# Kernel tuning notes

Measured on AMD Instinct MI355X. Metric: run time of the kernel, lower is better.

## Reference

```python
import jax, jax.numpy as jnp
import numpy as np

NUM_HEADS = 16
HEAD_DIM = 128
NUM_KV_HEADS = 8
NUM_KV_GROUPS = 2
HIDDEN = 2048
SCALE = 0.5  # hardcoded in the original SDPA call


def _fixed_sincos_pos(E, H):
    # matches ReusedProjReconstructor._fixed_sincos_pos (H even here)
    half = H // 2
    freq = jnp.exp(-jnp.log(jnp.float32(10000.0)) * jnp.arange(half, dtype=jnp.float32) / half)
    pos = jnp.arange(E, dtype=jnp.float32)[:, None]
    ang = pos * freq[None, :]
    return jnp.concatenate([jnp.sin(ang), jnp.cos(ang)], axis=1)  # [E, H]


def setup_inputs() -> dict:
    key = jax.random.key(0)
    ks = jax.random.split(key, 8)
    B, M, H = 4, 2048, HIDDEN
    kv_dim = NUM_KV_HEADS * HEAD_DIM
    s = 0.02
    return {
        "mem_act": jax.random.normal(ks[0], (B, M, H), jnp.float32),
        "Wq": jax.random.normal(ks[1], (H, H), jnp.float32) * s,
        "bq": jax.random.normal(ks[2], (H,), jnp.float32) * s,
        "Wk": jax.random.normal(ks[3], (kv_dim, H), jnp.float32) * s,
        "bk": jax.random.normal(ks[4], (kv_dim,), jnp.float32) * s,
        "Wv": jax.random.normal(ks[5], (kv_dim, H), jnp.float32) * s,
        "bv": jax.random.normal(ks[6], (kv_dim,), jnp.float32) * s,
        "Wo": jax.random.normal(ks[7], (H, H), jnp.float32) * s,
        "E": 2048,
    }


def reference(mem_act, Wq, bq, Wk, bk, Wv, bv, Wo, E):
    B, M, H = mem_act.shape
    # positional query hidden, shared across batch (q_ln is Identity)
    q_hidden = _fixed_sincos_pos(E, H).astype(mem_act.dtype)  # [E, H]
    q = (q_hidden @ Wq.T + bq).reshape(E, NUM_HEADS, HEAD_DIM)          # [E, nh, hd]
    k = (mem_act @ Wk.T + bk).reshape(B, M, NUM_KV_HEADS, HEAD_DIM)     # [B, M, nkv, hd]
    v = (mem_act @ Wv.T + bv).reshape(B, M, NUM_KV_HEADS, HEAD_DIM)
    # GQA: repeat kv heads (repeat_interleave over head dim)
    k = jnp.repeat(k, NUM_KV_GROUPS, axis=2)  # [B, M, nh, hd]
    v = jnp.repeat(v, NUM_KV_GROUPS, axis=2)
    # non-causal SDPA with scale=0.5, query broadcast over batch
    scores = jnp.einsum("ehd,bmhd->bhem", q, k) * SCALE  # [B, nh, E, M]
    attn = jax.nn.softmax(scores, axis=-1)
    out = jnp.einsum("bhem,bmhd->behd", attn, v).reshape(B, E, H)
    pred = out @ Wo.T  # o_proj (no bias, Qwen2 style)
    return pred
```

## Files before the change

kernel.cpp:

```cpp
#include <hip/hip_runtime.h>
#include <hip/hip_bf16.h>

typedef __attribute__((ext_vector_type(8))) short short8;
typedef __attribute__((ext_vector_type(4))) float f32x4;
typedef __attribute__((ext_vector_type(16))) float f32x16;
typedef unsigned short ushort_t;

__device__ __forceinline__ unsigned short f2bf(float x) {
    unsigned int u = __builtin_bit_cast(unsigned int, x);
    unsigned int r = (u + 0x7fffu + ((u >> 16) & 1u)) >> 16;
    return (unsigned short)r;
}

__device__ __forceinline__ void gload_lds16(const ushort_t* g, ushort_t* l) {
    __builtin_amdgcn_global_load_lds(
        (const __attribute__((address_space(1))) void*)g,
        (__attribute__((address_space(3))) void*)l, 16, 0, 0);
}

#define MFMA16(A, B, C) __builtin_amdgcn_mfma_f32_16x16x32_bf16((A), (B), (C), 0, 0, 0)
#define MFMA32(A, B, C) __builtin_amdgcn_mfma_f32_32x32x16_bf16((A), (B), (C), 0, 0, 0)

__global__ __launch_bounds__(256) void cvt_all(const float* __restrict__ im,
                                               const float* __restrict__ iq,
                                               const float* __restrict__ ik,
                                               const float* __restrict__ iv,
                                               const float* __restrict__ io,
                                               ushort_t* __restrict__ om,
                                               ushort_t* __restrict__ oq,
                                               ushort_t* __restrict__ ok,
                                               ushort_t* __restrict__ ov,
                                               ushort_t* __restrict__ oo) {
    long i = ((long)blockIdx.x * 256 + threadIdx.x) << 3;
    const float* s;
    ushort_t* d;
    if (i < 16777216)      { s = im + i;              d = om + i; }
    else if (i < 20971520) { s = iq + (i - 16777216); d = oq + (i - 16777216); }
    else if (i < 23068672) { s = ik + (i - 20971520); d = ok + (i - 20971520); }
    else if (i < 25165824) { s = iv + (i - 23068672); d = ov + (i - 23068672); }
    else                   { s = io + (i - 25165824); d = oo + (i - 25165824); }
    const float4* p = (const float4*)s;
    float4 a = p[0], b = p[1];
    short8 o;
    o[0] = (short)f2bf(a.x); o[1] = (short)f2bf(a.y);
    o[2] = (short)f2bf(a.z); o[3] = (short)f2bf(a.w);
    o[4] = (short)f2bf(b.x); o[5] = (short)f2bf(b.y);
    o[6] = (short)f2bf(b.z); o[7] = (short)f2bf(b.w);
    *(short8*)d = o;
}

__global__ __launch_bounds__(256) void fill_qh(ushort_t* __restrict__ qh) {
    int idx = blockIdx.x * 256 + threadIdx.x;
    int e = idx >> 10, i = idx & 1023;
    float freq = __expf(-9.2103403719761836f * (float)i * (1.0f / 1024.0f));
    float ang = (float)e * freq;
    qh[(size_t)e * 2048 + i]        = f2bf(sinf(ang));
    qh[(size_t)e * 2048 + 1024 + i] = f2bf(cosf(ang));
}

__global__ __launch_bounds__(256) void gemm_q(const ushort_t* __restrict__ A,
                                              const ushort_t* __restrict__ Bw,
                                              const float* __restrict__ bias,
                                              ushort_t* __restrict__ Cout,
                                              int M, int N, int K) {
    __shared__ ushort_t As[128 * 32];
    __shared__ ushort_t Bs[128 * 32];
    const int tid = threadIdx.x;
    const int lane = tid & 63;
    const int wid = tid >> 6;
    const int g = lane >> 4;
    const int r = lane & 15;
    const int wr = wid >> 1, wc = wid & 1;
    const int nbn = N >> 7;
    const int bm = blockIdx.x / nbn, bn = blockIdx.x % nbn;
    const int row0 = bm << 7, col0 = bn << 7;

    f32x4 acc[4][4];
#pragma unroll
    for (int i = 0; i < 4; ++i)
#pragma unroll
        for (int j = 0; j < 4; ++j) acc[i][j] = (f32x4){0.f, 0.f, 0.f, 0.f};

    const int f0 = tid * 8;
    const int r0_ = f0 >> 5, c0_ = f0 & 31;
    const int f1 = (256 + tid) * 8;
    const int r1_ = f1 >> 5, c1_ = f1 & 31;

    for (int k0 = 0; k0 < K; k0 += 32) {
        __syncthreads();
        gload_lds16(A  + (size_t)(row0 + r0_) * K + k0 + c0_, As + f0);
        gload_lds16(A  + (size_t)(row0 + r1_) * K + k0 + c1_, As + f1);
        gload_lds16(Bw + (size_t)(col0 + r0_) * K + k0 + c0_, Bs + f0);
        gload_lds16(Bw + (size_t)(col0 + r1_) * K + k0 + c1_, Bs + f1);
        __syncthreads();
        short8 af[4], bfr[4];
#pragma unroll
        for (int i = 0; i < 4; ++i) {
            af[i]  = *(const short8*)(As + (wr * 64 + i * 16 + r) * 32 + g * 8);
            bfr[i] = *(const short8*)(Bs + (wc * 64 + i * 16 + r) * 32 + g * 8);
        }
#pragma unroll
        for (int i = 0; i < 4; ++i)
#pragma unroll
            for (int j = 0; j < 4; ++j) acc[i][j] = MFMA16(af[i], bfr[j], acc[i][j]);
    }

#pragma unroll
    for (int j = 0; j < 4; ++j) {
        const int col = col0 + wc * 64 + j * 16 + r;
        const float bv = bias[col];
#pragma unroll
        for (int i = 0; i < 4; ++i) {
            const int rowb = row0 + wr * 64 + i * 16 + g * 4;
#pragma unroll
            for (int t = 0; t < 4; ++t) {
                float v = (acc[i][j][t] + bv) * 0.5f;
                Cout[(size_t)(rowb + t) * N + col] = f2bf(v);
            }
        }
    }
}

template <int EPI>
__global__ __launch_bounds__(512, 1) void gemm256(const ushort_t* __restrict__ A,
                                                  const ushort_t* __restrict__ Bw,
                                                  const float* __restrict__ b0,
                                                  const float* __restrict__ b1,
                                                  void* __restrict__ C0,
                                                  void* __restrict__ C1,
                                                  int M, int N, int K) {
    __shared__ ushort_t As[3][256 * 32];
    __shared__ ushort_t Bs[3][256 * 32];
    const int tid = threadIdx.x, lane = tid & 63;
    const int wid = tid >> 6;
    const int q5 = lane & 31, hi = lane >> 5;
    const int wm = wid >> 2, wn = wid & 3;
    const int nbn = N >> 8;
    const int nwg = gridDim.x;
    const int swz = (blockIdx.x & 7) * (nwg >> 3) + (blockIdx.x >> 3);
    const int bm = swz / nbn, bn = swz % nbn;
    const int row0 = bm << 8, col0 = bn << 8;
    const int NT = K >> 5;

    f32x16 acc[4][2];
#pragma unroll
    for (int mi = 0; mi < 4; ++mi)
#pragma unroll
        for (int nj = 0; nj < 2; ++nj)
#pragma unroll
            for (int rr = 0; rr < 16; ++rr) acc[mi][nj][rr] = 0.f;

    auto STAGE_HALF = [&](int buf, int kt, int i) {
        const int k0 = kt << 5;
        const int fb = (i * 512 + tid) << 4;
        const int rp = fb >> 7;
        const int bo = ((fb >> 4) & 7) ^ (rp & 7);
        const int row = rp * 2 + (bo >> 2);
        const int kc = (bo & 3) << 3;
        gload_lds16(A  + (size_t)(row0 + row) * K + k0 + kc, &As[buf][0] + (fb >> 1));
        gload_lds16(Bw + (size_t)(col0 + row) * K + k0 + kc, &Bs[buf][0] + (fb >> 1));
    };

    STAGE_HALF(0, 0, 0); STAGE_HALF(0, 0, 1);
    STAGE_HALF(1, 1, 0); STAGE_HALF(1, 1, 1);
    asm volatile("s_waitcnt vmcnt(4)" ::: "memory");
    __builtin_amdgcn_sched_barrier(0);
    __builtin_amdgcn_s_barrier();
    __builtin_amdgcn_sched_barrier(0);

    for (int t = 0; t < NT; ++t) {
        const int buf = t % 3;
        const char* Ab = (const char*)&As[buf][0];
        const char* Bb = (const char*)&Bs[buf][0];
#pragma unroll
        for (int ph = 0; ph < 2; ++ph) {
            short8 af[4], bfr[2];
#pragma unroll
            for (int nj = 0; nj < 2; ++nj) {
                const int col = wn * 64 + nj * 32 + q5;
                const int rp = col >> 1;
                const int blk = (((col & 1) << 2) + ph * 2 + hi) ^ (rp & 7);
                bfr[nj] = *(const short8*)(Bb + rp * 128 + blk * 16);
            }
#pragma unroll
            for (int mi = 0; mi < 4; ++mi) {
                const int row = wm * 128 + mi * 32 + q5;
                const int rp = row >> 1;
                const int blk = (((row & 1) << 2) + ph * 2 + hi) ^ (rp & 7);
                af[mi] = *(const short8*)(Ab + rp * 128 + blk * 16);
            }
            if (t + 2 < NT) STAGE_HALF((t + 2) % 3, t + 2, ph);
            __builtin_amdgcn_s_setprio(1);
#pragma unroll
            for (int mi = 0; mi < 4; ++mi)
#pragma unroll
                for (int nj = 0; nj < 2; ++nj)
                    acc[mi][nj] = MFMA32(af[mi], bfr[nj], acc[mi][nj]);
            __builtin_amdgcn_s_setprio(0);
            if (ph == 0) {
                __builtin_amdgcn_sched_barrier(0);
                __builtin_amdgcn_s_barrier();
                __builtin_amdgcn_sched_barrier(0);
            }
        }

        if (t + 2 < NT) {
            asm volatile("s_waitcnt vmcnt(4)" ::: "memory");
        } else if (t + 1 < NT) {
            asm volatile("s_waitcnt vmcnt(0)" ::: "memory");
        }
        if (t + 1 < NT) {
            __builtin_amdgcn_sched_barrier(0);
            __builtin_amdgcn_s_barrier();
            __builtin_amdgcn_sched_barrier(0);
        }
    }

#pragma unroll
    for (int mi = 0; mi < 4; ++mi)
#pragma unroll
        for (int nj = 0; nj < 2; ++nj) {
            const int col = col0 + wn * 64 + nj * 32 + q5;
            if (EPI == 2) {
                float* outp = (float*)C0;
#pragma unroll
                for (int rr = 0; rr < 16; ++rr) {
                    const int row = row0 + wm * 128 + mi * 32 + (rr & 3) + 8 * (rr >> 2) + 4 * hi;
                    outp[(size_t)row * N + col] = acc[mi][nj][rr];
                }
            } else {
                if (col < 1024) {
                    const float bv = b0[col];
                    ushort_t* Kp = (ushort_t*)C0;
#pragma unroll
                    for (int rr = 0; rr < 16; ++rr) {
                        const int row = row0 + wm * 128 + mi * 32 + (rr & 3) + 8 * (rr >> 2) + 4 * hi;
                        Kp[(size_t)row * 1024 + col] = f2bf(acc[mi][nj][rr] + bv);
                    }
                } else {
                    const int vcol = col - 1024;
                    const float bv = b1[vcol];
                    ushort_t* Vt = (ushort_t*)C1;
#pragma unroll
                    for (int G = 0; G < 4; ++G) {
                        const int m0 = row0 + wm * 128 + mi * 32 + G * 8 + 4 * hi;
                        const int bb = m0 >> 11;
                        const int mm = m0 & 2047;
                        const size_t vtrow = (size_t)(bb * 8 + (vcol >> 7)) * 128 + (vcol & 127);
                        unsigned int p0 = (unsigned int)f2bf(acc[mi][nj][G * 4 + 0] + bv)
                                        | ((unsigned int)f2bf(acc[mi][nj][G * 4 + 1] + bv) << 16);
                        unsigned int p1 = (unsigned int)f2bf(acc[mi][nj][G * 4 + 2] + bv)
                                        | ((unsigned int)f2bf(acc[mi][nj][G * 4 + 3] + bv) << 16);
                        uint2 pk; pk.x = p0; pk.y = p1;
                        *(uint2*)(Vt + vtrow * 2048 + mm) = pk;
                    }
                }
            }
        }
}

__global__ __launch_bounds__(512, 2) void attn_kernel(const ushort_t* __restrict__ Q,
                                                      const ushort_t* __restrict__ Kg,
                                                      const ushort_t* __restrict__ Vt,
                                                      ushort_t* __restrict__ O) {
    __shared__ ushort_t Ks[2][64 * 128];
    __shared__ ushort_t Vts[2][128 * 64];

    const int tid = threadIdx.x, lane = tid & 63, wid = tid >> 6;
    const int q5 = lane & 31;
    const int hi = lane >> 5;
    const int wq = wid & 3;
    const int wg = (blockIdx.x & 7) * 64 + (blockIdx.x >> 3);
    const int bkvh = wg >> 4;
    const int etile = wg & 15;
    const int b = bkvh >> 3, kvh = bkvh & 7;
    const int h = kvh * 2 + (wid >> 2);
    const int e0 = etile * 128;
    const int qrow = e0 + wq * 32 + q5;

    short8 Qf[8];
    {
        const ushort_t* qp = Q + (size_t)qrow * 2048 + h * 128 + hi * 8;
#pragma unroll
        for (int c = 0; c < 8; ++c) Qf[c] = *(const short8*)(qp + c * 16);
    }

    float mrow = -1e30f, lrow = 0.f;
    f32x16 oacc[4];
#pragma unroll
    for (int d0 = 0; d0 < 4; ++d0)
#pragma unroll
        for (int r = 0; r < 16; ++r) oacc[d0][r] = 0.f;

    const ushort_t* Kbase  = Kg + (size_t)b * 2048 * 1024 + kvh * 128;
    const ushort_t* Vtbase = Vt + (size_t)bkvh * 128 * 2048;

    auto STAGE = [&](int buf, int kv0) {
#pragma unroll
        for (int i = 0; i < 2; ++i) {
            const int fb = (i * 8 + wid) * 1024 + lane * 16;
            const int key = fb >> 8;
            const int blk = (fb >> 4) & 15;
            gload_lds16(Kbase + (size_t)(kv0 + key) * 1024 + ((blk ^ (key & 7)) << 3),
                        &Ks[buf][0] + (fb >> 1));
            const int d = fb >> 7;
            const int kb = (fb >> 4) & 7;
            gload_lds16(Vtbase + (size_t)d * 2048 + kv0 + ((kb ^ (d & 7)) << 3),
                        &Vts[buf][0] + (fb >> 1));
        }
    };

    STAGE(0, 0);
    __syncthreads();
    int cur = 0;

    for (int t = 0; t < 32; ++t) {
        if (t < 31) STAGE(cur ^ 1, (t + 1) * 64);
        const char* ks = (const char*)&Ks[cur][0];
        const char* vs = (const char*)&Vts[cur][0];

        f32x16 sS[2];
#pragma unroll
        for (int h2 = 0; h2 < 2; ++h2)
#pragma unroll
            for (int r = 0; r < 16; ++r) sS[h2][r] = 0.f;
#pragma unroll
        for (int h2 = 0; h2 < 2; ++h2) {
            const int key = h2 * 32 + q5;
            const int ksw = key & 7;
#pragma unroll
            for (int c = 0; c < 8; ++c) {
                short8 ka = *(const short8*)(ks + key * 256 + (((c * 2 + hi) ^ ksw) << 4));
                sS[h2] = MFMA32(ka, Qf[c], sS[h2]);
            }
        }

        float vm = fmaxf(sS[0][0], sS[0][1]);
#pragma unroll
        for (int r = 2; r < 16; ++r) vm = fmaxf(vm, sS[0][r]);
#pragma unroll
        for (int r = 0; r < 16; ++r) vm = fmaxf(vm, sS[1][r]);
        vm = fmaxf(vm, __shfl_xor(vm, 32));

        if (__any(vm > mrow + 8.0f)) {
            const float mn = fmaxf(mrow, vm);
            const float esc = __expf(mrow - mn);
            mrow = mn;
            lrow *= esc;
#pragma unroll
            for (int reg = 0; reg < 16; ++reg) {
                const float er = __shfl(esc, (reg & 3) + 8 * (reg >> 2) + 4 * hi);
#pragma unroll
                for (int d0 = 0; d0 < 4; ++d0) oacc[d0][reg] *= er;
            }
        }

        float rs = 0.f;
#pragma unroll
        for (int h2 = 0; h2 < 2; ++h2)
#pragma unroll
            for (int r = 0; r < 16; ++r) {
                const float p = __expf(sS[h2][r] - mrow);
                sS[h2][r] = p;
                rs += p;
            }
        rs += __shfl_xor(rs, 32);
        lrow += rs;

        unsigned int W[2][4][2], Wsw[2][4][2];
#pragma unroll
        for (int h2 = 0; h2 < 2; ++h2)
#pragma unroll
            for (int q4 = 0; q4 < 4; ++q4)
#pragma unroll
                for (int p = 0; p < 2; ++p) {
                    unsigned int w;
                    asm("v_cvt_pk_bf16_f32 %0, %1, %2"
                        : "=v"(w)
                        : "v"(sS[h2][q4 * 4 + 2 * p]), "v"(sS[h2][q4 * 4 + 2 * p + 1]));
                    W[h2][q4][p] = w;
                    Wsw[h2][q4][p] = __shfl_xor(w, 32);
                }

#pragma unroll
        for (int c16 = 0; c16 < 4; ++c16) {
            const int h2 = c16 >> 1;
            const int q4a = (c16 & 1) * 2, q4b = q4a + 1;
            union { unsigned int w[4]; short8 v; } pa;
            pa.w[0] = hi ? Wsw[h2][q4b][0] : W[h2][q4a][0];
            pa.w[1] = hi ? Wsw[h2][q4b][1] : W[h2][q4a][1];
            pa.w[2] = hi ? W[h2][q4b][0] : Wsw[h2][q4a][0];
            pa.w[3] = hi ? W[h2][q4b][1] : Wsw[h2][q4a][1];
#pragma unroll
            for (int d0 = 0; d0 < 4; ++d0) {
                const int d = d0 * 32 + q5;
                short8 vb = *(const short8*)(vs + d * 128 + (((c16 * 2 + hi) ^ (d & 7)) << 4));
                oacc[d0] = MFMA32(pa.v, vb, oacc[d0]);
            }
        }

        __syncthreads();
        cur ^= 1;
    }

#pragma unroll
    for (int reg = 0; reg < 16; ++reg) {
        const int qr = (reg & 3) + 8 * (reg >> 2) + 4 * hi;
        const float lr = __shfl(lrow, qr);
        const float inv = 1.0f / lr;
        const int e = e0 + wq * 32 + qr;
        ushort_t* op = O + ((size_t)b * 2048 + e) * 2048 + h * 128 + q5;
#pragma unroll
        for (int d0 = 0; d0 < 4; ++d0)
            op[d0 * 32] = f2bf(oacc[d0][reg] * inv);
    }
}

extern "C" void kernel_launch(void* const* d_in, const int* in_sizes, int n_in,
                              void* d_out, int out_size, void* d_ws, size_t ws_size,
                              hipStream_t stream) {
    const float* mem_act = (const float*)d_in[0];
    const float* Wq = (const float*)d_in[1];
    const float* bq = (const float*)d_in[2];
    const float* Wk = (const float*)d_in[3];
    const float* bk = (const float*)d_in[4];
    const float* Wv = (const float*)d_in[5];
    const float* bv = (const float*)d_in[6];
    const float* Wo = (const float*)d_in[7];
    float* out = (float*)d_out;

    char* w = (char*)d_ws;
    ushort_t* memb = (ushort_t*)w; w += (size_t)16777216 * 2;
    ushort_t* wqb  = (ushort_t*)w; w += (size_t)4194304 * 2;
    ushort_t* wkvb = (ushort_t*)w; w += (size_t)4194304 * 2;
    ushort_t* wob  = (ushort_t*)w; w += (size_t)4194304 * 2;
    ushort_t* qh   = (ushort_t*)w; w += (size_t)4194304 * 2;
    ushort_t* Qp   = (ushort_t*)w; w += (size_t)4194304 * 2;
    ushort_t* Kp   = (ushort_t*)w; w += (size_t)8388608 * 2;
    ushort_t* Vtp  = (ushort_t*)w; w += (size_t)8388608 * 2;
    ushort_t* AO   = (ushort_t*)w; w += (size_t)16777216 * 2;

    dim3 blk(256);
    cvt_all<<<14336, blk, 0, stream>>>(mem_act, Wq, Wk, Wv, Wo,
                                       memb, wqb, wkvb, wkvb + (size_t)2097152, wob);
    fill_qh<<<(2048 * 1024) / 256, blk, 0, stream>>>(qh);

    gemm_q<<<16 * 16, blk, 0, stream>>>(qh, wqb, bq, Qp, 2048, 2048, 2048);

    gemm256<0><<<256, dim3(512), 0, stream>>>(memb, wkvb, bk, bv, Kp, Vtp, 8192, 2048, 2048);

    attn_kernel<<<512, dim3(512), 0, stream>>>(Qp, Kp, Vtp, AO);

    gemm256<2><<<256, dim3(512), 0, stream>>>(AO, wob, nullptr, nullptr, out, nullptr, 8192, 2048, 2048);
}
```

Measured before the change: 404.3 us.

## Use permlane32_swap for P fragments, tree reductions, setprio around MFMA blocks

Replaces the ds_bpermute-based __shfl_xor lane swaps used to build the P operand with the gfx950 permlane32_swap intrinsic, which exchanges halves of the wave in registers. The row max and row sum reductions become balanced trees instead of serial chains, which shortens dependency latency. The QK^T loop is reordered to interleave the two key halves, and the first MFMA now takes a zero accumulator instead of an explicit clear. s_setprio hints bracket the MFMA regions so waves issuing matrix work get priority. The intent is to cut LDS shuffle traffic and VALU latency in the flash-attention inner loop. The risk is register pressure or scheduling changes that hurt overlap.

```diff
diff --git a/kernel.cpp b/kernel.cpp
--- a/kernel.cpp
+++ b/kernel.cpp
@@ -292,6 +292,10 @@
 #pragma unroll
         for (int r = 0; r < 16; ++r) oacc[d0][r] = 0.f;
 
+    f32x16 Z16;
+#pragma unroll
+    for (int r = 0; r < 16; ++r) Z16[r] = 0.f;
+
     const ushort_t* Kbase  = Kg + (size_t)b * 2048 * 1024 + kvh * 128;
     const ushort_t* Vtbase = Vt + (size_t)bkvh * 128 * 2048;
 
@@ -320,26 +324,28 @@
         const char* vs = (const char*)&Vts[cur][0];
 
         f32x16 sS[2];
-#pragma unroll
-        for (int h2 = 0; h2 < 2; ++h2)
-#pragma unroll
-            for (int r = 0; r < 16; ++r) sS[h2][r] = 0.f;
-#pragma unroll
-        for (int h2 = 0; h2 < 2; ++h2) {
-            const int key = h2 * 32 + q5;
-            const int ksw = key & 7;
-#pragma unroll
-            for (int c = 0; c < 8; ++c) {
-                short8 ka = *(const short8*)(ks + key * 256 + (((c * 2 + hi) ^ ksw) << 4));
-                sS[h2] = MFMA32(ka, Qf[c], sS[h2]);
-            }
-        }
-
-        float vm = fmaxf(sS[0][0], sS[0][1]);
-#pragma unroll
-        for (int r = 2; r < 16; ++r) vm = fmaxf(vm, sS[0][r]);
-#pragma unroll
-        for (int r = 0; r < 16; ++r) vm = fmaxf(vm, sS[1][r]);
+        __builtin_amdgcn_s_setprio(1);
+#pragma unroll
+        for (int c = 0; c < 8; ++c) {
+#pragma unroll
+            for (int h2 = 0; h2 < 2; ++h2) {
+                const int key = h2 * 32 + q5;
+                short8 ka = *(const short8*)(ks + key * 256 + (((c * 2 + hi) ^ (key & 7)) << 4));
+                sS[h2] = MFMA32(ka, Qf[c], (c == 0) ? Z16 : sS[h2]);
+            }
+        }
+        __builtin_amdgcn_s_setprio(0);
+
+        float tm[16];
+#pragma unroll
+        for (int i = 0; i < 8; ++i) tm[i] = fmaxf(sS[0][2 * i], sS[0][2 * i + 1]);
+#pragma unroll
+        for (int i = 0; i < 8; ++i) tm[8 + i] = fmaxf(sS[1][2 * i], sS[1][2 * i + 1]);
+#pragma unroll
+        for (int s = 8; s > 0; s >>= 1)
+#pragma unroll
+            for (int i = 0; i < s; ++i) tm[i] = fmaxf(tm[i], tm[i + s]);
+        float vm = tm[0];
         vm = fmaxf(vm, __shfl_xor(vm, 32));
 
         if (__any(vm > mrow + 8.0f)) {
@@ -355,19 +361,27 @@
             }
         }
 
-        float rs = 0.f;
+        float ts[16];
 #pragma unroll
         for (int h2 = 0; h2 < 2; ++h2)
 #pragma unroll
             for (int r = 0; r < 16; ++r) {
                 const float p = __expf(sS[h2][r] - mrow);
                 sS[h2][r] = p;
-                rs += p;
-            }
+            }
+#pragma unroll
+        for (int i = 0; i < 8; ++i) ts[i] = sS[0][2 * i] + sS[0][2 * i + 1];
+#pragma unroll
+        for (int i = 0; i < 8; ++i) ts[8 + i] = sS[1][2 * i] + sS[1][2 * i + 1];
+#pragma unroll
+        for (int s = 8; s > 0; s >>= 1)
+#pragma unroll
+            for (int i = 0; i < s; ++i) ts[i] = ts[i] + ts[i + s];
+        float rs = ts[0];
         rs += __shfl_xor(rs, 32);
         lrow += rs;
 
-        unsigned int W[2][4][2], Wsw[2][4][2];
+        unsigned int W[2][4][2];
 #pragma unroll
         for (int h2 = 0; h2 < 2; ++h2)
 #pragma unroll
@@ -379,24 +393,27 @@
                         : "=v"(w)
                         : "v"(sS[h2][q4 * 4 + 2 * p]), "v"(sS[h2][q4 * 4 + 2 * p + 1]));
                     W[h2][q4][p] = w;
-                    Wsw[h2][q4][p] = __shfl_xor(w, 32);
                 }
 
 #pragma unroll
         for (int c16 = 0; c16 < 4; ++c16) {
             const int h2 = c16 >> 1;
             const int q4a = (c16 & 1) * 2, q4b = q4a + 1;
+            auto r0 = __builtin_amdgcn_permlane32_swap(W[h2][q4a][0], W[h2][q4b][0], false, false);
+            auto r1 = __builtin_amdgcn_permlane32_swap(W[h2][q4a][1], W[h2][q4b][1], false, false);
             union { unsigned int w[4]; short8 v; } pa;
-            pa.w[0] = hi ? Wsw[h2][q4b][0] : W[h2][q4a][0];
-            pa.w[1] = hi ? Wsw[h2][q4b][1] : W[h2][q4a][1];
-            pa.w[2] = hi ? W[h2][q4b][0] : Wsw[h2][q4a][0];
-            pa.w[3] = hi ? W[h2][q4b][1] : Wsw[h2][q4a][1];
+            pa.w[0] = r0[0];
+            pa.w[1] = r1[0];
+            pa.w[2] = r0[1];
+            pa.w[3] = r1[1];
+            __builtin_amdgcn_s_setprio(1);
 #pragma unroll
             for (int d0 = 0; d0 < 4; ++d0) {
                 const int d = d0 * 32 + q5;
                 short8 vb = *(const short8*)(vs + d * 128 + (((c16 * 2 + hi) ^ (d & 7)) << 4));
                 oacc[d0] = MFMA32(pa.v, vb, oacc[d0]);
             }
+            __builtin_amdgcn_s_setprio(0);
         }
 
         __syncthreads();
```

After: 404.9 us. No clear change (+0.1%).
